# Performance work log

Hardware: AMD Instinct MI355X
Metric: run time of the kernel (lower is better)

Reference implementation:

```python
import jax, jax.numpy as jnp
import numpy as np

B, T, V, E, H = 4096, 128, 30, 256, 128

def setup_inputs() -> dict:
    key = jax.random.key(0)
    ks = jax.random.split(key, 12)
    inpt = jax.random.randint(ks[0], (B, T), 0, V, dtype=jnp.int32)
    h0 = jax.random.normal(ks[1], (B, H), dtype=jnp.float32)
    c0 = jax.random.normal(ks[2], (B, H), dtype=jnp.float32)
    mask_Y = jnp.ones((B, T), dtype=jnp.float32)
    s_e = 1.0
    s_l = 1.0 / np.sqrt(H)
    s_i = 1.0 / np.sqrt(E)
    emb = jax.random.normal(ks[3], (V, E), dtype=jnp.float32) * s_e
    W_ih = jax.random.normal(ks[4], (4 * H, E), dtype=jnp.float32) * s_i
    b_ih = jax.random.normal(ks[5], (4 * H,), dtype=jnp.float32) * s_i
    W_hh = jax.random.normal(ks[6], (4 * H, H), dtype=jnp.float32) * s_l
    b_hh = jax.random.normal(ks[7], (4 * H,), dtype=jnp.float32) * s_l
    W_lin = jax.random.normal(ks[8], (V, H), dtype=jnp.float32) * s_l
    b_lin = jax.random.normal(ks[9], (V,), dtype=jnp.float32) * s_l
    return {"inpt": inpt, "h0": h0, "c0": c0, "mask_Y": mask_Y, "beta": 1,
            "emb": emb, "W_ih": W_ih, "b_ih": b_ih, "W_hh": W_hh,
            "b_hh": b_hh, "W_lin": W_lin, "b_lin": b_lin}


def reference(inpt, h0, c0, mask_Y, beta, emb, W_ih, b_ih, W_hh, b_hh, W_lin, b_lin):
    # beta == 1 -> teacher forcing every step (u <= beta always), as in source.
    t_max = inpt.shape[1]
    # input tokens fed at steps t=0..t_max-2 are inpt[:, 0:t_max-1]
    x_emb = emb[inpt[:, :t_max - 1]]          # [B, T-1, E]
    xs = (jnp.swapaxes(x_emb, 0, 1),           # [T-1, B, E]
          inpt[:, 1:].T,                       # [T-1, B] true labels
          mask_Y[:, :t_max - 1].T)             # [T-1, B]

    def step(carry, xs_t):
        h, c = carry
        x, y, m = xs_t
        gates = x @ W_ih.T + b_ih + h @ W_hh.T + b_hh   # [B, 4H]
        i, f, g, o = jnp.split(gates, 4, axis=1)
        c2 = jax.nn.sigmoid(f) * c + jax.nn.sigmoid(i) * jnp.tanh(g)
        h2 = jax.nn.sigmoid(o) * jnp.tanh(c2)
        # -log(softmax(logits))[y] == -log_softmax(logits)[y]
        logp = jax.nn.log_softmax(h2 @ W_lin.T + b_lin, axis=1)  # [B, V]
        ce = -jnp.take_along_axis(logp, y[:, None], axis=1)[:, 0]
        return (h2, c2), jnp.sum(ce * m)

    _, step_losses = jax.lax.scan(step, (h0, c0), xs)
    return jnp.sum(step_losses) / jnp.sum(mask_Y)
```

## Files before the change

kernel.cpp:

```cpp
#include <hip/hip_runtime.h>


typedef __bf16 bf16x8 __attribute__((ext_vector_type(8)));
typedef float  f32x4  __attribute__((ext_vector_type(4)));

namespace {
constexpr int Bn = 4096, Tn = 128, Vn = 30, En = 256, Hn = 128, Gn = 512;
constexpr int WS_LOSS  = 0;
constexpr int WS_MASK  = 1;
constexpr int WS_CNT   = 2;
constexpr int WS_XPROJ = 16;
constexpr int WS_WF_F  = WS_XPROJ + Vn * Gn;
}

__device__ __forceinline__ float fexp2(float x) { return __builtin_amdgcn_exp2f(x); }
__device__ __forceinline__ float frcp(float x)  { return __builtin_amdgcn_rcpf(x); }
__device__ __forceinline__ float sigf(float x)  { return frcp(1.f + fexp2(x * -1.44269504f)); }
__device__ __forceinline__ float tanh_(float x) { return 1.f - 2.f * frcp(fexp2(x * 2.88539008f) + 1.f); }

__device__ __forceinline__ void lds_barrier() {
  __builtin_amdgcn_sched_barrier(0);
  asm volatile("s_waitcnt lgkmcnt(0)" ::: "memory");
  __builtin_amdgcn_s_barrier();
  __builtin_amdgcn_sched_barrier(0);
}

__global__ void k_setup(const float* __restrict__ emb, const float* __restrict__ W_ih,
                        const float* __restrict__ b_ih, const float* __restrict__ b_hh,
                        const float* __restrict__ W_hh, const float* __restrict__ W_lin,
                        float* __restrict__ ws) {
  const int bid = blockIdx.x, tid = threadIdx.x;
  if (bid < 60) {
    __shared__ __align__(16) float es[En];
    int v = bid >> 1;
    int j = ((bid & 1) << 8) + tid;
    es[tid] = emb[v * En + tid];
    __syncthreads();
    float a = b_ih[j] + b_hh[j];
    const float* wr = W_ih + j * En;
#pragma unroll 4
    for (int e = 0; e < En; e += 4) {
      float4 w = *(const float4*)(wr + e);
      float4 x = *(const float4*)(es + e);
      a += x.x * w.x + x.y * w.y + x.z * w.z + x.w * w.w;
    }
    ws[WS_XPROJ + v * Gn + (j & 127) * 4 + (j >> 7)] = a;
  } else if (bid < 92) {
    int fid = (bid - 60) * 256 + tid;
    int l = fid & 63, kt = (fid >> 6) & 3, g = (fid >> 8) & 3, w = fid >> 10;
    int n  = (g * 8 + w) * 16 + (l & 15);
    int k0 = kt * 32 + (l >> 4) * 8;
    const float* src = W_hh + n * Hn + k0;
    union { __bf16 h[8]; uint4 u; } pk;
#pragma unroll
    for (int j = 0; j < 8; ++j) pk.h[j] = (__bf16)src[j];
    __bf16* wf = (__bf16*)(ws + WS_WF_F);
    *(uint4*)(wf + fid * 8) = pk.u;
  } else {
    int fid = (bid - 92) * 256 + tid;
    if (fid < 3) ws[fid] = 0.f;
    int l = fid & 63, kt = (fid >> 6) & 3, n = fid >> 8;
    int col = n * 16 + (l & 15);
    int k0  = kt * 32 + (l >> 4) * 8;
    union { __bf16 h[8]; uint4 u; } pk;
#pragma unroll
    for (int j = 0; j < 8; ++j)
      pk.h[j] = (col < Vn) ? (__bf16)W_lin[col * Hn + k0 + j] : (__bf16)0.f;
    __bf16* wf = (__bf16*)(ws + WS_WF_F);
    *(uint4*)(wf + 65536 + fid * 8) = pk.u;
  }
}

__global__ __launch_bounds__(512, 1) void k_main(
    const int* __restrict__ inpt, const float* __restrict__ h0,
    const float* __restrict__ c0, const float* __restrict__ maskY,
    const float* __restrict__ b_lin, float* __restrict__ ws,
    float* __restrict__ out) {
  __shared__ __align__(16) __bf16 hbuf[2][16][136];
  __shared__ int   tokL[16 * 129];
  __shared__ float maskL[16 * 132];
  __shared__ __align__(16) float logitsL[2][16 * 36];
  __shared__ float red[2];

  const float4* X4 = (const float4*)(ws + WS_XPROJ);
  const __bf16* wf  = (const __bf16*)(ws + WS_WF_F);
  const __bf16* wlf = wf + 65536;

  const int tid = threadIdx.x;
  const int w = tid >> 6, l = tid & 63, quad = l >> 4, lc = l & 15;
  const int row0 = blockIdx.x * 16;
  const int kh = w * 16 + lc;

  for (int idx = tid; idx < 16 * Tn; idx += 512) {
    int r = idx >> 7, t = idx & 127;
    tokL[r * 129 + t]  = inpt[(row0 + r) * Tn + t];
    maskL[r * 132 + t] = maskY[(row0 + r) * Tn + t];
  }
  for (int idx = tid; idx < 16 * Hn; idx += 512) {
    int r = idx >> 7, k = idx & 127;
    hbuf[0][r][k] = (__bf16)h0[(row0 + r) * Hn + k];
  }

  bf16x8 wreg[4][4];
  bf16x8 wlin[4];
  float  creg[4];
  float  blin = 0.f, mloc = 0.f, ce_acc = 0.f;

#pragma unroll
  for (int g = 0; g < 4; ++g)
#pragma unroll
    for (int kt = 0; kt < 4; ++kt)
      wreg[g][kt] = __builtin_bit_cast(
          bf16x8, *(const uint4*)(wf + (((w * 4 + g) * 4 + kt) * 64 + l) * 8));
#pragma unroll
  for (int p = 0; p < 4; ++p)
    creg[p] = c0[(row0 + quad * 4 + p) * Hn + kh];

  if (w == 7) {
    float s = 0.f;
    const float4* m4 = (const float4*)(maskY + row0 * Tn);
#pragma unroll
    for (int i = 0; i < 8; ++i) s += m4[l + i * 64].x + m4[l + i * 64].y +
                                     m4[l + i * 64].z + m4[l + i * 64].w;
    mloc = s;
  }
  if (w < 2) {
#pragma unroll
    for (int kt = 0; kt < 4; ++kt)
      wlin[kt] = __builtin_bit_cast(
          bf16x8, *(const uint4*)(wlf + ((w * 4 + kt) * 64 + l) * 8));
    blin = (w == 0) ? b_lin[lc] : ((lc < Vn - 16) ? b_lin[16 + lc] : -1e30f);
  }
  __syncthreads();

  float4 xv[4];
#pragma unroll
  for (int p = 0; p < 4; ++p)
    xv[p] = X4[tokL[(quad * 4 + p) * 129] * 128 + kh];

  for (int t = 0; t <= Tn; ++t) {
    const int par = t & 1;
    const __bf16* hc = &hbuf[par][0][0];
    __bf16*       hn = &hbuf[par ^ 1][0][0];

    bf16x8 af[4];
    const bool have_af = (t < Tn - 1) || (w < 2 && t < Tn);
    if (have_af) {
#pragma unroll
      for (int kt = 0; kt < 4; ++kt)
        af[kt] = __builtin_bit_cast(
            bf16x8, *(const uint4*)(hc + lc * 136 + kt * 32 + quad * 8));
    }

    if (t < Tn - 1) {
      int tk[4];
#pragma unroll
      for (int p = 0; p < 4; ++p) tk[p] = tokL[(quad * 4 + p) * 129 + t + 1];

      f32x4 acc[4];
#pragma unroll
      for (int p = 0; p < 4; ++p) {
        acc[0][p] = xv[p].x; acc[1][p] = xv[p].y;
        acc[2][p] = xv[p].z; acc[3][p] = xv[p].w;
      }
#pragma unroll
      for (int g = 0; g < 4; ++g)
#pragma unroll
        for (int kt = 0; kt < 4; ++kt)
          acc[g] = __builtin_amdgcn_mfma_f32_16x16x32_bf16(af[kt], wreg[g][kt], acc[g], 0, 0, 0);

      float4 xn[4];
#pragma unroll
      for (int p = 0; p < 4; ++p) xn[p] = X4[tk[p] * 128 + kh];

#pragma unroll
      for (int p = 0; p < 4; ++p) {
        float c2 = sigf(acc[1][p]) * creg[p] + sigf(acc[0][p]) * tanh_(acc[2][p]);
        float h2 = sigf(acc[3][p]) * tanh_(c2);
        creg[p] = c2;
        hn[(quad * 4 + p) * 136 + kh] = (__bf16)h2;
        xv[p] = xn[p];
      }
    }

    if (w < 2 && t >= 1 && t < Tn) {
      f32x4 lacc = {blin, blin, blin, blin};
#pragma unroll
      for (int kt = 0; kt < 4; ++kt)
        lacc = __builtin_amdgcn_mfma_f32_16x16x32_bf16(af[kt], wlin[kt], lacc, 0, 0, 0);
#pragma unroll
      for (int p = 0; p < 4; ++p)
        logitsL[par][(quad * 4 + p) * 36 + kh] = lacc[p];
    }

    if ((w == 2 || w == 3) && t >= 2) {
      int srow = (w - 2) * 8 + (l >> 3);
      int j = l & 7;
      const float* Lr = &logitsL[par ^ 1][srow * 36];
      float4 v = *(const float4*)(Lr + j * 4);
      float m = fmaxf(fmaxf(v.x, v.y), fmaxf(v.z, v.w));
      m = fmaxf(m, __shfl_xor(m, 1));
      m = fmaxf(m, __shfl_xor(m, 2));
      m = fmaxf(m, __shfl_xor(m, 4));
      float e = fexp2((v.x - m) * 1.44269504f) + fexp2((v.y - m) * 1.44269504f) +
                fexp2((v.z - m) * 1.44269504f) + fexp2((v.w - m) * 1.44269504f);
      e += __shfl_xor(e, 1);
      e += __shfl_xor(e, 2);
      e += __shfl_xor(e, 4);
      if (j == 0) {
        int   y  = tokL[srow * 129 + t - 1];
        float ly = Lr[y];
        float ce = (m + __logf(e)) - ly;
        ce_acc += ce * maskL[srow * 132 + t - 2];
      }
    }
    lds_barrier();
  }

  if (w == 7) {
#pragma unroll
    for (int off = 32; off > 0; off >>= 1) mloc += __shfl_down(mloc, off);
    if (l == 0) red[0] = mloc;
  }
  if (w == 3) {
#pragma unroll
    for (int off = 32; off > 0; off >>= 1) ce_acc += __shfl_down(ce_acc, off);
    if (l == 0) red[1] = ce_acc;
  }
  __syncthreads();
  if (w == 2) {
#pragma unroll
    for (int off = 32; off > 0; off >>= 1) ce_acc += __shfl_down(ce_acc, off);
    if (l == 0) {
      atomicAdd(ws + WS_LOSS, ce_acc + red[1]);
      atomicAdd(ws + WS_MASK, red[0]);
      __threadfence();
      unsigned old = atomicAdd((unsigned*)(ws + WS_CNT), 1u);
      if (old == 255) {
        float lv = atomicAdd(ws + WS_LOSS, 0.f);
        float mv = atomicAdd(ws + WS_MASK, 0.f);
        out[0] = lv / mv;
      }
    }
  }
}

extern "C" void kernel_launch(void* const* d_in, const int* in_sizes, int n_in,
                              void* d_out, int out_size, void* d_ws, size_t ws_size,
                              hipStream_t stream) {
  const int*   inpt  = (const int*)  d_in[0];
  const float* h0    = (const float*)d_in[1];
  const float* c0    = (const float*)d_in[2];
  const float* maskY = (const float*)d_in[3];
  const float* emb   = (const float*)d_in[5];
  const float* W_ih  = (const float*)d_in[6];
  const float* b_ih  = (const float*)d_in[7];
  const float* W_hh  = (const float*)d_in[8];
  const float* b_hh  = (const float*)d_in[9];
  const float* W_lin = (const float*)d_in[10];
  const float* b_lin = (const float*)d_in[11];
  float* ws  = (float*)d_ws;
  float* out = (float*)d_out;

  hipLaunchKernelGGL(k_setup, dim3(94),  dim3(256), 0, stream,
                     emb, W_ih, b_ih, b_hh, W_hh, W_lin, ws);
  hipLaunchKernelGGL(k_main,  dim3(256), dim3(512), 0, stream,
                     inpt, h0, c0, maskY, b_lin, ws, out);
}
```

Baseline: 234.1 us.

## Move output projection and softmax to four dedicated extra wavefronts

```diff
diff --git a/kernel.cpp b/kernel.cpp
--- a/kernel.cpp
+++ b/kernel.cpp
@@ -71,7 +71,7 @@
   }
 }
 
-__global__ __launch_bounds__(512, 1) void k_main(
+__global__ __launch_bounds__(768, 1) void k_main(
     const int* __restrict__ inpt, const float* __restrict__ h0,
     const float* __restrict__ c0, const float* __restrict__ maskY,
     const float* __restrict__ b_lin, float* __restrict__ ws,
@@ -80,7 +80,7 @@
   __shared__ int   tokL[16 * 129];
   __shared__ float maskL[16 * 132];
   __shared__ __align__(16) float logitsL[2][16 * 36];
-  __shared__ float red[2];
+  __shared__ float red[4];
 
   const float4* X4 = (const float4*)(ws + WS_XPROJ);
   const __bf16* wf  = (const __bf16*)(ws + WS_WF_F);
@@ -91,12 +91,12 @@
   const int row0 = blockIdx.x * 16;
   const int kh = w * 16 + lc;
 
-  for (int idx = tid; idx < 16 * Tn; idx += 512) {
+  for (int idx = tid; idx < 16 * Tn; idx += 768) {
     int r = idx >> 7, t = idx & 127;
     tokL[r * 129 + t]  = inpt[(row0 + r) * Tn + t];
     maskL[r * 132 + t] = maskY[(row0 + r) * Tn + t];
   }
-  for (int idx = tid; idx < 16 * Hn; idx += 512) {
+  for (int idx = tid; idx < 16 * Hn; idx += 768) {
     int r = idx >> 7, k = idx & 127;
     hbuf[0][r][k] = (__bf16)h0[(row0 + r) * Hn + k];
   }
@@ -106,112 +106,118 @@
   float  creg[4];
   float  blin = 0.f, mloc = 0.f, ce_acc = 0.f;
 
-#pragma unroll
-  for (int g = 0; g < 4; ++g)
-#pragma unroll
-    for (int kt = 0; kt < 4; ++kt)
-      wreg[g][kt] = __builtin_bit_cast(
-          bf16x8, *(const uint4*)(wf + (((w * 4 + g) * 4 + kt) * 64 + l) * 8));
-#pragma unroll
-  for (int p = 0; p < 4; ++p)
-    creg[p] = c0[(row0 + quad * 4 + p) * Hn + kh];
-
-  if (w == 7) {
-    float s = 0.f;
-    const float4* m4 = (const float4*)(maskY + row0 * Tn);
-#pragma unroll
-    for (int i = 0; i < 8; ++i) s += m4[l + i * 64].x + m4[l + i * 64].y +
-                                     m4[l + i * 64].z + m4[l + i * 64].w;
-    mloc = s;
-  }
-  if (w < 2) {
+  if (w < 8) {
+#pragma unroll
+    for (int g = 0; g < 4; ++g)
+#pragma unroll
+      for (int kt = 0; kt < 4; ++kt)
+        wreg[g][kt] = __builtin_bit_cast(
+            bf16x8, *(const uint4*)(wf + (((w * 4 + g) * 4 + kt) * 64 + l) * 8));
+#pragma unroll
+    for (int p = 0; p < 4; ++p)
+      creg[p] = c0[(row0 + quad * 4 + p) * Hn + kh];
+    if (w == 7) {
+      float s = 0.f;
+      const float4* m4 = (const float4*)(maskY + row0 * Tn);
+#pragma unroll
+      for (int i = 0; i < 8; ++i) s += m4[l + i * 64].x + m4[l + i * 64].y +
+                                       m4[l + i * 64].z + m4[l + i * 64].w;
+      mloc = s;
+    }
+  } else if (w < 10) {
+    int n = w - 8;
 #pragma unroll
     for (int kt = 0; kt < 4; ++kt)
       wlin[kt] = __builtin_bit_cast(
-          bf16x8, *(const uint4*)(wlf + ((w * 4 + kt) * 64 + l) * 8));
-    blin = (w == 0) ? b_lin[lc] : ((lc < Vn - 16) ? b_lin[16 + lc] : -1e30f);
+          bf16x8, *(const uint4*)(wlf + ((n * 4 + kt) * 64 + l) * 8));
+    blin = (n == 0) ? b_lin[lc] : ((lc < Vn - 16) ? b_lin[16 + lc] : -1e30f);
   }
   __syncthreads();
 
   float4 xv[4];
-#pragma unroll
-  for (int p = 0; p < 4; ++p)
-    xv[p] = X4[tokL[(quad * 4 + p) * 129] * 128 + kh];
+  if (w < 8) {
+#pragma unroll
+    for (int p = 0; p < 4; ++p)
+      xv[p] = X4[tokL[(quad * 4 + p) * 129] * 128 + kh];
+  }
 
   for (int t = 0; t <= Tn; ++t) {
     const int par = t & 1;
     const __bf16* hc = &hbuf[par][0][0];
     __bf16*       hn = &hbuf[par ^ 1][0][0];
 
-    bf16x8 af[4];
-    const bool have_af = (t < Tn - 1) || (w < 2 && t < Tn);
-    if (have_af) {
-#pragma unroll
-      for (int kt = 0; kt < 4; ++kt)
-        af[kt] = __builtin_bit_cast(
-            bf16x8, *(const uint4*)(hc + lc * 136 + kt * 32 + quad * 8));
-    }
-
-    if (t < Tn - 1) {
-      int tk[4];
-#pragma unroll
-      for (int p = 0; p < 4; ++p) tk[p] = tokL[(quad * 4 + p) * 129 + t + 1];
-
-      f32x4 acc[4];
-#pragma unroll
-      for (int p = 0; p < 4; ++p) {
-        acc[0][p] = xv[p].x; acc[1][p] = xv[p].y;
-        acc[2][p] = xv[p].z; acc[3][p] = xv[p].w;
-      }
-#pragma unroll
-      for (int g = 0; g < 4; ++g)
+    if (w < 8) {
+      if (t < Tn - 1) {
+        bf16x8 af[4];
 #pragma unroll
         for (int kt = 0; kt < 4; ++kt)
-          acc[g] = __builtin_amdgcn_mfma_f32_16x16x32_bf16(af[kt], wreg[g][kt], acc[g], 0, 0, 0);
-
-      float4 xn[4];
-#pragma unroll
-      for (int p = 0; p < 4; ++p) xn[p] = X4[tk[p] * 128 + kh];
-
-#pragma unroll
-      for (int p = 0; p < 4; ++p) {
-        float c2 = sigf(acc[1][p]) * creg[p] + sigf(acc[0][p]) * tanh_(acc[2][p]);
-        float h2 = sigf(acc[3][p]) * tanh_(c2);
-        creg[p] = c2;
-        hn[(quad * 4 + p) * 136 + kh] = (__bf16)h2;
-        xv[p] = xn[p];
-      }
-    }
-
-    if (w < 2 && t >= 1 && t < Tn) {
-      f32x4 lacc = {blin, blin, blin, blin};
-#pragma unroll
-      for (int kt = 0; kt < 4; ++kt)
-        lacc = __builtin_amdgcn_mfma_f32_16x16x32_bf16(af[kt], wlin[kt], lacc, 0, 0, 0);
-#pragma unroll
-      for (int p = 0; p < 4; ++p)
-        logitsL[par][(quad * 4 + p) * 36 + kh] = lacc[p];
-    }
-
-    if ((w == 2 || w == 3) && t >= 2) {
-      int srow = (w - 2) * 8 + (l >> 3);
-      int j = l & 7;
-      const float* Lr = &logitsL[par ^ 1][srow * 36];
-      float4 v = *(const float4*)(Lr + j * 4);
-      float m = fmaxf(fmaxf(v.x, v.y), fmaxf(v.z, v.w));
-      m = fmaxf(m, __shfl_xor(m, 1));
-      m = fmaxf(m, __shfl_xor(m, 2));
-      m = fmaxf(m, __shfl_xor(m, 4));
-      float e = fexp2((v.x - m) * 1.44269504f) + fexp2((v.y - m) * 1.44269504f) +
-                fexp2((v.z - m) * 1.44269504f) + fexp2((v.w - m) * 1.44269504f);
-      e += __shfl_xor(e, 1);
-      e += __shfl_xor(e, 2);
-      e += __shfl_xor(e, 4);
-      if (j == 0) {
-        int   y  = tokL[srow * 129 + t - 1];
-        float ly = Lr[y];
-        float ce = (m + __logf(e)) - ly;
-        ce_acc += ce * maskL[srow * 132 + t - 2];
+          af[kt] = __builtin_bit_cast(
+              bf16x8, *(const uint4*)(hc + lc * 136 + kt * 32 + quad * 8));
+
+        int tk[4];
+#pragma unroll
+        for (int p = 0; p < 4; ++p) tk[p] = tokL[(quad * 4 + p) * 129 + t + 1];
+
+        f32x4 acc[4];
+#pragma unroll
+        for (int p = 0; p < 4; ++p) {
+          acc[0][p] = xv[p].x; acc[1][p] = xv[p].y;
+          acc[2][p] = xv[p].z; acc[3][p] = xv[p].w;
+        }
+#pragma unroll
+        for (int g = 0; g < 4; ++g)
+#pragma unroll
+          for (int kt = 0; kt < 4; ++kt)
+            acc[g] = __builtin_amdgcn_mfma_f32_16x16x32_bf16(af[kt], wreg[g][kt], acc[g], 0, 0, 0);
+
+        float4 xn[4];
+#pragma unroll
+        for (int p = 0; p < 4; ++p) xn[p] = X4[tk[p] * 128 + kh];
+
+#pragma unroll
+        for (int p = 0; p < 4; ++p) {
+          float c2 = sigf(acc[1][p]) * creg[p] + sigf(acc[0][p]) * tanh_(acc[2][p]);
+          float h2 = sigf(acc[3][p]) * tanh_(c2);
+          creg[p] = c2;
+          hn[(quad * 4 + p) * 136 + kh] = (__bf16)h2;
+          xv[p] = xn[p];
+        }
+      }
+    } else {
+      if (w < 10 && t >= 1 && t < Tn) {
+        bf16x8 af[4];
+#pragma unroll
+        for (int kt = 0; kt < 4; ++kt)
+          af[kt] = __builtin_bit_cast(
+              bf16x8, *(const uint4*)(hc + lc * 136 + kt * 32 + quad * 8));
+        f32x4 lacc = {blin, blin, blin, blin};
+#pragma unroll
+        for (int kt = 0; kt < 4; ++kt)
+          lacc = __builtin_amdgcn_mfma_f32_16x16x32_bf16(af[kt], wlin[kt], lacc, 0, 0, 0);
+#pragma unroll
+        for (int p = 0; p < 4; ++p)
+          logitsL[par][(quad * 4 + p) * 36 + (w - 8) * 16 + lc] = lacc[p];
+      }
+      if (t >= 2) {
+        int srow = (w - 8) * 4 + quad;
+        const float* Lr = &logitsL[par ^ 1][srow * 36];
+        float2 v = *(const float2*)(Lr + lc * 2);
+        float m = fmaxf(v.x, v.y);
+        m = fmaxf(m, __shfl_xor(m, 1));
+        m = fmaxf(m, __shfl_xor(m, 2));
+        m = fmaxf(m, __shfl_xor(m, 4));
+        m = fmaxf(m, __shfl_xor(m, 8));
+        float e = fexp2((v.x - m) * 1.44269504f) + fexp2((v.y - m) * 1.44269504f);
+        e += __shfl_xor(e, 1);
+        e += __shfl_xor(e, 2);
+        e += __shfl_xor(e, 4);
+        e += __shfl_xor(e, 8);
+        if (lc == 0) {
+          int   y  = tokL[srow * 129 + t - 1];
+          float ly = Lr[y];
+          float ce = (m + __logf(e)) - ly;
+          ce_acc += ce * maskL[srow * 132 + t - 2];
+        }
       }
     }
     lds_barrier();
@@ -222,17 +228,17 @@
     for (int off = 32; off > 0; off >>= 1) mloc += __shfl_down(mloc, off);
     if (l == 0) red[0] = mloc;
   }
-  if (w == 3) {
+  if (w >= 9) {
 #pragma unroll
     for (int off = 32; off > 0; off >>= 1) ce_acc += __shfl_down(ce_acc, off);
-    if (l == 0) red[1] = ce_acc;
+    if (l == 0) red[w - 8] = ce_acc;
   }
   __syncthreads();
-  if (w == 2) {
+  if (w == 8) {
 #pragma unroll
     for (int off = 32; off > 0; off >>= 1) ce_acc += __shfl_down(ce_acc, off);
     if (l == 0) {
-      atomicAdd(ws + WS_LOSS, ce_acc + red[1]);
+      atomicAdd(ws + WS_LOSS, ce_acc + red[1] + red[2] + red[3]);
       atomicAdd(ws + WS_MASK, red[0]);
       __threadfence();
       unsigned old = atomicAdd((unsigned*)(ws + WS_CNT), 1u);
@@ -264,6 +270,6 @@
 
   hipLaunchKernelGGL(k_setup, dim3(94),  dim3(256), 0, stream,
                      emb, W_ih, b_ih, b_hh, W_hh, W_lin, ws);
-  hipLaunchKernelGGL(k_main,  dim3(256), dim3(512), 0, stream,
+  hipLaunchKernelGGL(k_main,  dim3(256), dim3(768), 0, stream,
                      inpt, h0, c0, maskY, b_lin, ws, out);
 }
```

New measurement: 236.1 us. No clear change (+0.8%).
